# Performance work log

Hardware: AMD Instinct MI355X
Metric: run time of the kernel (lower is better)

The kernel has to match this reference:

```python
import jax, jax.numpy as jnp
import numpy as np

B, C, H, W = 8, 512, 32, 32
NUM_HEADS = 8
WINDOW = 32
L = H * W
BN_EPS = 1e-5


def setup_inputs() -> dict:
    key = jax.random.key(0)
    ks = jax.random.split(key, 8)
    s = lambda k, shape, sc=0.02: jax.random.normal(k, shape, jnp.float32) * sc
    return {
        "x": jax.random.normal(ks[0], (B, C, H, W), jnp.float32),
        "dw_weight": s(ks[1], (C, 1, 3, 3), 0.1),
        "dw_bias": jnp.zeros((C,), jnp.float32),
        "shared_weight": s(ks[2], (1, 1, 3, 3), 0.3),
        "shared_bias": jnp.zeros((1,), jnp.float32),
        "mix_weight": jnp.float32(0.7),
        "bn_gamma": jnp.ones((C,), jnp.float32),
        "bn_beta": jnp.zeros((C,), jnp.float32),
        "det_w1": s(ks[3], (C // 4, 2 * C)),
        "det_b1": jnp.zeros((C // 4,), jnp.float32),
        "det_w2": s(ks[4], (1, C // 4)),
        "det_b2": jnp.zeros((1,), jnp.float32),
        "in_proj_w": s(ks[5], (3 * C, C)),
        "in_proj_b": jnp.zeros((3 * C,), jnp.float32),
        "out_proj_w": s(ks[6], (C, C)),
        "out_proj_b": jnp.zeros((C,), jnp.float32),
    }


def _circ_pad(x):
    # F.pad(x, (1,1,1,1), mode='circular')
    return jnp.pad(x, ((0, 0), (0, 0), (1, 1), (1, 1)), mode="wrap")


def _dw_conv(xp, w, b):
    # depthwise 3x3, VALID on circularly padded input
    out = jax.lax.conv_general_dilated(
        xp, w, window_strides=(1, 1), padding="VALID",
        dimension_numbers=("NCHW", "OIHW", "NCHW"), feature_group_count=C)
    return out + b[None, :, None, None]


def _local_mask():
    # True = blocked; row i allows columns [i - WINDOW//2, i + WINDOW//2]
    i = jnp.arange(L)[:, None]
    j = jnp.arange(L)[None, :]
    allowed = (j >= i - WINDOW // 2) & (j <= i + WINDOW // 2)
    return ~allowed


def _forward(x, dw_weight, dw_bias, shared_weight, shared_bias, mix_weight,
             bn_gamma, bn_beta, det_w1, det_b1, det_w2, det_b2,
             in_proj_w, in_proj_b, out_proj_w, out_proj_b):
    # --- DualWalze (eval mode: BN uses running_mean=0, running_var=1) ---
    xp = _circ_pad(x)
    main_out = _dw_conv(xp, dw_weight, dw_bias)
    shared_kernel = jnp.broadcast_to(shared_weight, (C, 1, 3, 3))
    shared_b = jnp.broadcast_to(shared_bias, (C,))
    express_out = _dw_conv(xp, shared_kernel, shared_b)
    mix = jax.nn.sigmoid(mix_weight)
    combined = mix * main_out + (1.0 - mix) * express_out + x  # residual
    bn = bn_gamma[None, :, None, None] * combined * jax.lax.rsqrt(jnp.float32(1.0 + BN_EPS)) \
         + bn_beta[None, :, None, None]
    x_walze = jax.nn.gelu(bn, approximate=False)  # (B, C, H, W)

    # --- AdaptiveSpikeDetectorV3 (eval: no history, temp = 1.0) ---
    x_before_seq = x.transpose(0, 2, 3, 1).reshape(B, L, C)
    x_after_seq = x_walze.transpose(0, 2, 3, 1).reshape(B, L, C)
    comb = jnp.concatenate([x_before_seq, x_after_seq], axis=-1)  # (B, L, 2C)
    h = jax.nn.gelu(jnp.einsum("blf,kf->blk", comb, det_w1) + det_b1, approximate=False)
    spike_logits = jnp.einsum("blk,ok->blo", h, det_w2) + det_b2  # (B, L, 1)
    soft_mask = jax.nn.sigmoid(spike_logits)  # temperature 1.0 at progress 0
    soft_mask = soft_mask.reshape(B, H, W, 1).transpose(0, 3, 1, 2)  # (B,1,H,W)

    # --- AttentionWithMemory: windowed MHA over flattened sequence ---
    seq = x_after_seq  # (B, L, C)
    qkv = jnp.einsum("blc,fc->blf", seq, in_proj_w) + in_proj_b
    q, k, v = jnp.split(qkv, 3, axis=-1)
    hd = C // NUM_HEADS
    to_heads = lambda t: t.reshape(B, L, NUM_HEADS, hd).transpose(0, 2, 1, 3)
    q, k, v = to_heads(q), to_heads(k), to_heads(v)
    scores = jnp.einsum("bhqd,bhkd->bhqk", q, k) / jnp.sqrt(jnp.float32(hd))
    scores = jnp.where(_local_mask()[None, None], jnp.float32(-1e30), scores)
    attn = jax.nn.softmax(scores, axis=-1)
    ctx = jnp.einsum("bhqk,bhkd->bhqd", attn, v)
    ctx = ctx.transpose(0, 2, 1, 3).reshape(B, L, C)
    attn_out = jnp.einsum("blc,oc->blo", ctx, out_proj_w) + out_proj_b
    attn_spatial = attn_out.reshape(B, H, W, C).transpose(0, 3, 1, 2)

    # --- gated residual combine ---
    return x_walze + soft_mask * attn_spatial


def reference(x, dw_weight, dw_bias, shared_weight, shared_bias, mix_weight,
              bn_gamma, bn_beta, det_w1, det_b1, det_w2, det_b2,
              in_proj_w, in_proj_b, out_proj_w, out_proj_b):
    return _forward(x, dw_weight, dw_bias, shared_weight, shared_bias, mix_weight,
                    bn_gamma, bn_beta, det_w1, det_b1, det_w2, det_b2,
                    in_proj_w, in_proj_b, out_proj_w, out_proj_b)
```

## Files before the change

### kernel.cpp

```cpp
#include <hip/hip_runtime.h>

#define B_ 8
#define C_ 512
#define H_ 32
#define W_ 32
#define L_ 1024
#define M_ 8192
#define NH_ 8
#define HD_ 64

typedef float f32x4 __attribute__((ext_vector_type(4)));
typedef short s16x8 __attribute__((ext_vector_type(8)));

__device__ __forceinline__ f32x4 mfma_bf16(f32x4 acc, s16x8 a, s16x8 b) {
    asm("v_mfma_f32_16x16x32_bf16 %0, %1, %2, %0" : "+v"(acc) : "v"(a), "v"(b));
    return acc;
}

__device__ __forceinline__ s16x8 ldg8(const unsigned short* p) {
    return *(const s16x8*)p;
}

typedef __attribute__((address_space(1))) const unsigned int glob_u32;
typedef __attribute__((address_space(3))) unsigned int lds_u32;
__device__ __forceinline__ void async_cp16(const void* g, void* l) {
    __builtin_amdgcn_global_load_lds((glob_u32*)g, (lds_u32*)l, 16, 0, 0);
}

__device__ __forceinline__ unsigned short f2bf(float f) {
    unsigned int u = __float_as_uint(f);
    unsigned int r = (u + 0x7FFFu + ((u >> 16) & 1u)) >> 16;
    return (unsigned short)r;
}

__device__ __forceinline__ float bf2f(unsigned short u) {
    return __uint_as_float(((unsigned int)u) << 16);
}

__device__ __forceinline__ float gelu_exact(float v) {
    return 0.5f * v * (1.0f + erff(v * 0.70710678118654752f));
}

__device__ __forceinline__ float sigmoidf_(float v) {
    return 1.0f / (1.0f + __expf(-v));
}

__global__ __launch_bounds__(256) void k_cvt_weights(
        const float* __restrict__ w1, const float* __restrict__ w2,
        const float* __restrict__ w3,
        unsigned short* __restrict__ o1, unsigned short* __restrict__ o2,
        unsigned short* __restrict__ o3, int n1, int n2, int n3) {
    int i = blockIdx.x * 256 + threadIdx.x;
    if (i < n1) o1[i] = f2bf(w1[i]);
    if (i < n2) o2[i] = f2bf(w2[i]);
    if (i < n3) o3[i] = f2bf(w3[i]);
}

__global__ __launch_bounds__(256) void k_walze(
        const float* __restrict__ x, const float* __restrict__ dww,
        const float* __restrict__ dwb, const float* __restrict__ shw,
        const float* __restrict__ shb, const float* __restrict__ mixw,
        const float* __restrict__ gamma, const float* __restrict__ beta,
        float* __restrict__ xw) {
    __shared__ float tile[1024];
    int bc = blockIdx.x;
    int c = bc & (C_ - 1);
    int tid = threadIdx.x;
    const float* xp = x + (size_t)bc * 1024;
#pragma unroll
    for (int t = 0; t < 4; ++t) tile[tid + 256 * t] = xp[tid + 256 * t];
    __syncthreads();
    float wm[9], wsh[9];
#pragma unroll
    for (int t = 0; t < 9; ++t) { wm[t] = dww[c * 9 + t]; wsh[t] = shw[t]; }
    float mix = sigmoidf_(mixw[0]);
    float bmain = dwb[c], bsh = shb[0];
    float g = gamma[c], bt = beta[c];
    const float rs = rsqrtf(1.0f + 1e-5f);
#pragma unroll
    for (int t = 0; t < 4; ++t) {
        int l = tid + 256 * t;
        int h = l >> 5, w = l & 31;
        float accm = 0.f, accs = 0.f;
#pragma unroll
        for (int kh = 0; kh < 3; ++kh) {
            int hh = (h + kh + 31) & 31;
#pragma unroll
            for (int kw = 0; kw < 3; ++kw) {
                int ww = (w + kw + 31) & 31;
                float v = tile[hh * 32 + ww];
                accm += v * wm[kh * 3 + kw];
                accs += v * wsh[kh * 3 + kw];
            }
        }
        float combined = mix * (accm + bmain) + (1.f - mix) * (accs + bsh) + tile[l];
        float bn = g * combined * rs + bt;
        xw[(size_t)bc * 1024 + l] = gelu_exact(bn);
    }
}

__global__ __launch_bounds__(256) void k_pack(
        const float* __restrict__ x, const float* __restrict__ xw,
        unsigned short* __restrict__ comb) {
    __shared__ float Tx[64 * 65];
    __shared__ float Tw[64 * 65];
    int b = blockIdx.z;
    int c0 = blockIdx.y * 64;
    int l0 = blockIdx.x * 64;
    int tid = threadIdx.x;
    for (int idx = tid; idx < 1024; idx += 256) {
        int cr = idx >> 4, f = idx & 15;
        size_t src = ((size_t)(b * C_ + c0 + cr) << 10) + l0 + f * 4;
        float4 vx = *(const float4*)(x + src);
        float4 vw = *(const float4*)(xw + src);
        *(float4*)&Tx[cr * 65 + f * 4] = vx;
        *(float4*)&Tw[cr * 65 + f * 4] = vw;
    }
    __syncthreads();
    for (int idx = tid; idx < 1024; idx += 256) {
        int lr = idx >> 4, f = idx & 15;
        ushort4 ux, uw;
        ux.x = f2bf(Tx[(4 * f + 0) * 65 + lr]);
        ux.y = f2bf(Tx[(4 * f + 1) * 65 + lr]);
        ux.z = f2bf(Tx[(4 * f + 2) * 65 + lr]);
        ux.w = f2bf(Tx[(4 * f + 3) * 65 + lr]);
        uw.x = f2bf(Tw[(4 * f + 0) * 65 + lr]);
        uw.y = f2bf(Tw[(4 * f + 1) * 65 + lr]);
        uw.z = f2bf(Tw[(4 * f + 2) * 65 + lr]);
        uw.w = f2bf(Tw[(4 * f + 3) * 65 + lr]);
        unsigned short* row = comb + (((size_t)(b << 10) + l0 + lr) << 10);
        *(ushort4*)(row + c0 + 4 * f) = ux;
        *(ushort4*)(row + 512 + c0 + 4 * f) = uw;
    }
}

__global__ __launch_bounds__(256) void k_detector(
        const unsigned short* __restrict__ comb, const unsigned short* __restrict__ w1,
        const float* __restrict__ b1, const float* __restrict__ w2,
        const float* __restrict__ b2, float* __restrict__ sm) {
    __shared__ float red[64];
    int tid = threadIdx.x;
    int wave = tid >> 6, lane = tid & 63;
    int col = lane & 15, quad = lane >> 4;
    int m0 = blockIdx.x * 16;
    int koff = quad * 8;
    int nb0 = wave * 32, nb1 = nb0 + 16;
    const unsigned short* pa  = comb + (size_t)(m0 + col) * 1024 + koff;
    const unsigned short* pw0 = w1 + (size_t)(nb0 + col) * 1024 + koff;
    const unsigned short* pw1 = w1 + (size_t)(nb1 + col) * 1024 + koff;
    f32x4 acc0 = {0.f, 0.f, 0.f, 0.f}, acc1 = {0.f, 0.f, 0.f, 0.f};
    for (int k = 0; k < 1024; k += 32) {
        s16x8 a = ldg8(pa + k);
        acc0 = mfma_bf16(acc0, a, ldg8(pw0 + k));
        acc1 = mfma_bf16(acc1, a, ldg8(pw1 + k));
    }
    asm volatile("s_nop 7\ns_nop 7");
    float bia0 = b1[nb0 + col], bia1 = b1[nb1 + col];
    float wv0 = w2[nb0 + col], wv1 = w2[nb1 + col];
#pragma unroll
    for (int r = 0; r < 4; ++r) {
        float h0 = gelu_exact(acc0[r] + bia0);
        float h1 = gelu_exact(acc1[r] + bia1);
        float p = h0 * wv0 + h1 * wv1;
        p += __shfl_xor(p, 1);
        p += __shfl_xor(p, 2);
        p += __shfl_xor(p, 4);
        p += __shfl_xor(p, 8);
        if (col == 0) red[wave * 16 + quad * 4 + r] = p;
    }
    __syncthreads();
    if (tid < 16) {
        float s = red[tid] + red[16 + tid] + red[32 + tid] + red[48 + tid] + b2[0];
        sm[m0 + tid] = sigmoidf_(s);
    }
}

__global__ __launch_bounds__(256) void k_gemm_qkv(
        const unsigned short* __restrict__ A,
        const unsigned short* __restrict__ Wt,
        const float* __restrict__ bias,
        unsigned short* __restrict__ out_hi, unsigned short* __restrict__ out_lo) {
    __shared__ unsigned short As[128 * 64];
    __shared__ unsigned short Bs[128 * 64];
    int tid = threadIdx.x;
    int wave = tid >> 6, lane = tid & 63;
    int col = lane & 15, quad = lane >> 4;
    int wr = wave & 1, wc = wave >> 1;
    int mb = blockIdx.y * 128, nb = blockIdx.x * 128;
    int srow = tid >> 3, sko = tid & 7;
    f32x4 acc[4][4] = {};
    for (int kb = 0; kb < 512; kb += 64) {
#pragma unroll
        for (int p = 0; p < 4; ++p) {
            int r = p * 32 + srow;
            async_cp16(A + (size_t)(mb + r) * 1024 + kb + sko * 8, &As[r * 64 + sko * 8]);
            async_cp16(Wt + (size_t)(nb + r) * 512 + kb + sko * 8, &Bs[r * 64 + sko * 8]);
        }
        __syncthreads();
#pragma unroll
        for (int ks = 0; ks < 64; ks += 32) {
            s16x8 a[4], b[4];
#pragma unroll
            for (int i = 0; i < 4; ++i)
                a[i] = *(const s16x8*)&As[(wr * 64 + i * 16 + col) * 64 + ks + quad * 8];
#pragma unroll
            for (int j = 0; j < 4; ++j)
                b[j] = *(const s16x8*)&Bs[(wc * 64 + j * 16 + col) * 64 + ks + quad * 8];
#pragma unroll
            for (int i = 0; i < 4; ++i)
#pragma unroll
                for (int j = 0; j < 4; ++j)
                    acc[i][j] = mfma_bf16(acc[i][j], a[i], b[j]);
        }
        __syncthreads();
    }
    asm volatile("s_nop 7\ns_nop 7");
#pragma unroll
    for (int i = 0; i < 4; ++i)
#pragma unroll
        for (int j = 0; j < 4; ++j) {
            int n = nb + wc * 64 + j * 16 + col;
            float bv = bias[n];
#pragma unroll
            for (int r = 0; r < 4; ++r) {
                int m = mb + wr * 64 + i * 16 + quad * 4 + r;
                float v = acc[i][j][r] + bv;
                unsigned short hi = f2bf(v);
                size_t idx = (size_t)m * 1536 + n;
                out_hi[idx] = hi;
                out_lo[idx] = f2bf(v - bf2f(hi));
            }
        }
}

__global__ __launch_bounds__(256) void k_attn(
        const unsigned short* __restrict__ qkv_hi,
        const unsigned short* __restrict__ qkv_lo,
        unsigned short* __restrict__ ctx) {
    __shared__ unsigned short Vth[64 * 104];
    __shared__ unsigned short Vtl[64 * 104];
    __shared__ unsigned short Ph[4][16 * 104];
    __shared__ unsigned short Pl[4][16 * 104];
    int b = blockIdx.z, h = blockIdx.y;
    int q0 = blockIdx.x * 64;
    int tid = threadIdx.x, wave = tid >> 6, lane = tid & 63;
    int col = lane & 15, quad = lane >> 4;
    int jlo_t = max(q0 - 16, 0);
    const unsigned short* baseh = qkv_hi + ((size_t)(b << 10)) * 1536;
    const unsigned short* basel = qkv_lo + ((size_t)(b << 10)) * 1536;
#pragma unroll
    for (int it = 0; it < 3; ++it) {
        int slot = it * 256 + tid;
        int kg = slot >> 6, d = slot & 63;
        int key0 = jlo_t + kg * 8;
        unsigned short eh[8], el[8];
#pragma unroll
        for (int t = 0; t < 8; ++t) {
            size_t ro = (size_t)min(key0 + t, 1023) * 1536 + 1024 + h * 64 + d;
            eh[t] = baseh[ro];
            el[t] = basel[ro];
        }
        ushort4 h0 = {eh[0], eh[1], eh[2], eh[3]}, h1 = {eh[4], eh[5], eh[6], eh[7]};
        ushort4 l0 = {el[0], el[1], el[2], el[3]}, l1 = {el[4], el[5], el[6], el[7]};
        *(ushort4*)&Vth[d * 104 + kg * 8] = h0;
        *(ushort4*)&Vth[d * 104 + kg * 8 + 4] = h1;
        *(ushort4*)&Vtl[d * 104 + kg * 8] = l0;
        *(ushort4*)&Vtl[d * 104 + kg * 8 + 4] = l1;
    }
    __syncthreads();
    size_t qoff = (size_t)(q0 + wave * 16 + col) * 1536 + h * 64;
    s16x8 aq0h = ldg8(baseh + qoff + quad * 8);
    s16x8 aq1h = ldg8(baseh + qoff + 32 + quad * 8);
    s16x8 aq0l = ldg8(basel + qoff + quad * 8);
    s16x8 aq1l = ldg8(basel + qoff + 32 + quad * 8);
    f32x4 S[6];
#pragma unroll
    for (int nt = 0; nt < 6; ++nt) {
        size_t koffb = (size_t)min(jlo_t + nt * 16 + col, 1023) * 1536 + 512 + h * 64;
        s16x8 kh0 = ldg8(baseh + koffb + quad * 8);
        s16x8 kh1 = ldg8(baseh + koffb + 32 + quad * 8);
        s16x8 kl0 = ldg8(basel + koffb + quad * 8);
        s16x8 kl1 = ldg8(basel + koffb + 32 + quad * 8);
        f32x4 z = {0.f, 0.f, 0.f, 0.f};
        z = mfma_bf16(z, aq0h, kh0);
        z = mfma_bf16(z, aq1h, kh1);
        z = mfma_bf16(z, aq0h, kl0);
        z = mfma_bf16(z, aq1h, kl1);
        z = mfma_bf16(z, aq0l, kh0);
        z = mfma_bf16(z, aq1l, kh1);
        S[nt] = z;
    }
    asm volatile("s_nop 7\ns_nop 7");
    int i_base = q0 + wave * 16 + quad * 4;
    float mx[4] = {-1e30f, -1e30f, -1e30f, -1e30f};
#pragma unroll
    for (int nt = 0; nt < 6; ++nt) {
        int j = jlo_t + nt * 16 + col;
#pragma unroll
        for (int r = 0; r < 4; ++r) {
            int i = i_base + r;
            bool ok = (j <= 1023) && (j >= i - 16) && (j <= i + 16);
            float s = ok ? S[nt][r] * 0.125f : -1e30f;
            S[nt][r] = s;
            mx[r] = fmaxf(mx[r], s);
        }
    }
#pragma unroll
    for (int r = 0; r < 4; ++r) {
        mx[r] = fmaxf(mx[r], __shfl_xor(mx[r], 1));
        mx[r] = fmaxf(mx[r], __shfl_xor(mx[r], 2));
        mx[r] = fmaxf(mx[r], __shfl_xor(mx[r], 4));
        mx[r] = fmaxf(mx[r], __shfl_xor(mx[r], 8));
    }
    float sum[4] = {0.f, 0.f, 0.f, 0.f};
#pragma unroll
    for (int nt = 0; nt < 6; ++nt)
#pragma unroll
        for (int r = 0; r < 4; ++r) {
            float p = __expf(S[nt][r] - mx[r]);
            S[nt][r] = p;
            sum[r] += p;
        }
#pragma unroll
    for (int r = 0; r < 4; ++r) {
        sum[r] += __shfl_xor(sum[r], 1);
        sum[r] += __shfl_xor(sum[r], 2);
        sum[r] += __shfl_xor(sum[r], 4);
        sum[r] += __shfl_xor(sum[r], 8);
        sum[r] = 1.f / sum[r];
    }
#pragma unroll
    for (int nt = 0; nt < 6; ++nt)
#pragma unroll
        for (int r = 0; r < 4; ++r) {
            float pv = S[nt][r] * sum[r];
            unsigned short hi = f2bf(pv);
            Ph[wave][(quad * 4 + r) * 104 + nt * 16 + col] = hi;
            Pl[wave][(quad * 4 + r) * 104 + nt * 16 + col] = f2bf(pv - bf2f(hi));
        }
    __syncthreads();
    f32x4 O[4] = {};
#pragma unroll
    for (int ks = 0; ks < 96; ks += 32) {
        s16x8 aph = *(const s16x8*)&Ph[wave][col * 104 + ks + quad * 8];
        s16x8 apl = *(const s16x8*)&Pl[wave][col * 104 + ks + quad * 8];
#pragma unroll
        for (int nt = 0; nt < 4; ++nt) {
            s16x8 bvh = *(const s16x8*)&Vth[(nt * 16 + col) * 104 + ks + quad * 8];
            s16x8 bvl = *(const s16x8*)&Vtl[(nt * 16 + col) * 104 + ks + quad * 8];
            O[nt] = mfma_bf16(O[nt], aph, bvh);
            O[nt] = mfma_bf16(O[nt], apl, bvh);
            O[nt] = mfma_bf16(O[nt], aph, bvl);
        }
    }
    asm volatile("s_nop 7\ns_nop 7");
#pragma unroll
    for (int nt = 0; nt < 4; ++nt)
#pragma unroll
        for (int r = 0; r < 4; ++r) {
            int i = i_base + r;
            ctx[((size_t)(b << 10) + i) * 512 + h * 64 + nt * 16 + col] = f2bf(O[nt][r]);
        }
}

__global__ __launch_bounds__(256) void k_out_combine(
        const unsigned short* __restrict__ Wt, const unsigned short* __restrict__ Actx,
        const float* __restrict__ bias, const float* __restrict__ xw,
        const float* __restrict__ sm, float* __restrict__ out) {
    __shared__ unsigned short As[128 * 64];
    __shared__ unsigned short Bs[128 * 64];
    int tid = threadIdx.x;
    int wave = tid >> 6, lane = tid & 63;
    int col = lane & 15, quad = lane >> 4;
    int wr = wave & 1, wc = wave >> 1;
    int mb = blockIdx.y * 128, nb = blockIdx.x * 128;
    int srow = tid >> 3, sko = tid & 7;
    f32x4 acc[4][4] = {};
    for (int kb = 0; kb < 512; kb += 64) {
#pragma unroll
        for (int p = 0; p < 4; ++p) {
            int r = p * 32 + srow;
            async_cp16(Wt + (size_t)(mb + r) * 512 + kb + sko * 8, &As[r * 64 + sko * 8]);
            async_cp16(Actx + (size_t)(nb + r) * 512 + kb + sko * 8, &Bs[r * 64 + sko * 8]);
        }
        __syncthreads();
#pragma unroll
        for (int ks = 0; ks < 64; ks += 32) {
            s16x8 a[4], b[4];
#pragma unroll
            for (int i = 0; i < 4; ++i)
                a[i] = *(const s16x8*)&As[(wr * 64 + i * 16 + col) * 64 + ks + quad * 8];
#pragma unroll
            for (int j = 0; j < 4; ++j)
                b[j] = *(const s16x8*)&Bs[(wc * 64 + j * 16 + col) * 64 + ks + quad * 8];
#pragma unroll
            for (int i = 0; i < 4; ++i)
#pragma unroll
                for (int j = 0; j < 4; ++j)
                    acc[i][j] = mfma_bf16(acc[i][j], a[i], b[j]);
        }
        __syncthreads();
    }
    asm volatile("s_nop 7\ns_nop 7");
#pragma unroll
    for (int i = 0; i < 4; ++i)
#pragma unroll
        for (int j = 0; j < 4; ++j) {
            int seq = nb + wc * 64 + j * 16 + col;
            int bb = seq >> 10, l = seq & 1023;
            float smv = sm[seq];
#pragma unroll
            for (int r = 0; r < 4; ++r) {
                int c = mb + wr * 64 + i * 16 + quad * 4 + r;
                float v = acc[i][j][r] + bias[c];
                size_t oidx = ((size_t)(bb * C_ + c) << 10) + l;
                out[oidx] = xw[oidx] + smv * v;
            }
        }
}

extern "C" void kernel_launch(void* const* d_in, const int* in_sizes, int n_in,
                              void* d_out, int out_size, void* d_ws, size_t ws_size,
                              hipStream_t stream) {
    const float* x      = (const float*)d_in[0];
    const float* dw_w   = (const float*)d_in[1];
    const float* dw_b   = (const float*)d_in[2];
    const float* sh_w   = (const float*)d_in[3];
    const float* sh_b   = (const float*)d_in[4];
    const float* mix_w  = (const float*)d_in[5];
    const float* bn_g   = (const float*)d_in[6];
    const float* bn_b   = (const float*)d_in[7];
    const float* det_w1 = (const float*)d_in[8];
    const float* det_b1 = (const float*)d_in[9];
    const float* det_w2 = (const float*)d_in[10];
    const float* det_b2 = (const float*)d_in[11];
    const float* inp_w  = (const float*)d_in[12];
    const float* inp_b  = (const float*)d_in[13];
    const float* outp_w = (const float*)d_in[14];
    const float* outp_b = (const float*)d_in[15];
    float* out = (float*)d_out;

    char* ws = (char*)d_ws;
    size_t off = 0;
    auto alloc = [&](size_t bytes) -> void* {
        void* p = ws + off;
        off += (bytes + 255) & ~(size_t)255;
        return p;
    };
    float* xw             = (float*)alloc((size_t)M_ * C_ * 4);
    unsigned short* comb  = (unsigned short*)alloc((size_t)M_ * 1024 * 2);
    unsigned short* qkvh  = (unsigned short*)alloc((size_t)M_ * 1536 * 2);
    unsigned short* qkvl  = (unsigned short*)alloc((size_t)M_ * 1536 * 2);
    unsigned short* ctx   = (unsigned short*)alloc((size_t)M_ * 512 * 2);
    float* smask          = (float*)alloc((size_t)M_ * 4);
    unsigned short* w1b   = (unsigned short*)alloc(131072 * 2);
    unsigned short* inwb  = (unsigned short*)alloc(786432 * 2);
    unsigned short* outwb = (unsigned short*)alloc(262144 * 2);
    (void)ws_size; (void)in_sizes; (void)n_in; (void)out_size;

    k_cvt_weights<<<3072, 256, 0, stream>>>(det_w1, inp_w, outp_w, w1b, inwb, outwb,
                                            131072, 786432, 262144);
    k_walze<<<B_ * C_, 256, 0, stream>>>(x, dw_w, dw_b, sh_w, sh_b, mix_w, bn_g, bn_b, xw);
    k_pack<<<dim3(16, 8, 8), 256, 0, stream>>>(x, xw, comb);
    k_detector<<<M_ / 16, 256, 0, stream>>>(comb, w1b, det_b1, det_w2, det_b2, smask);
    k_gemm_qkv<<<dim3(1536 / 128, M_ / 128), 256, 0, stream>>>(comb + 512, inwb, inp_b,
                                                               qkvh, qkvl);
    k_attn<<<dim3(16, NH_, B_), 256, 0, stream>>>(qkvh, qkvl, ctx);
    k_out_combine<<<dim3(M_ / 128, C_ / 128), 256, 0, stream>>>(outwb, ctx, outp_b,
                                                                xw, smask, out);
}
```

Baseline: 197.4 us.

## Fuse depthwise-conv walze with bf16 pack and widen detector to 8 waves

Merges the depthwise-conv/BN/GELU kernel with the transpose-and-pack kernel. Each block loads a 4-row by 64-channel tile with circular halo rows into LDS, computes the walze output per channel lane, writes the bf16 combined rows directly, and writes xw back through an LDS transpose. This removes one launch and the re-read of x and xw from global memory. Separately, the detector kernel now uses 512 threads, each wave owning one 16-column N tile instead of two, to increase parallelism. The fused kernel's per-lane 2-byte strided comb stores and 32-entry register array may limit coalescing and occupancy.

```diff
diff --git a/kernel.cpp b/kernel.cpp
--- a/kernel.cpp
+++ b/kernel.cpp
@@ -56,20 +56,39 @@
     if (i < n3) o3[i] = f2bf(w3[i]);
 }
 
-__global__ __launch_bounds__(256) void k_walze(
+__global__ __launch_bounds__(256) void k_walze_pack(
         const float* __restrict__ x, const float* __restrict__ dww,
         const float* __restrict__ dwb, const float* __restrict__ shw,
         const float* __restrict__ shb, const float* __restrict__ mixw,
         const float* __restrict__ gamma, const float* __restrict__ beta,
-        float* __restrict__ xw) {
-    __shared__ float tile[1024];
-    int bc = blockIdx.x;
-    int c = bc & (C_ - 1);
+        float* __restrict__ xw, unsigned short* __restrict__ comb) {
+    __shared__ float lds[64 * 193];
+    int h0 = blockIdx.x * 4;
+    int c0 = blockIdx.y * 64;
+    int b  = blockIdx.z;
     int tid = threadIdx.x;
-    const float* xp = x + (size_t)bc * 1024;
-#pragma unroll
-    for (int t = 0; t < 4; ++t) tile[tid + 256 * t] = xp[tid + 256 * t];
-    __syncthreads();
+    const float* xb = x + ((size_t)(b * C_ + c0) << 10);
+#pragma unroll
+    for (int k = 0; k < 8; ++k) {
+        int idx = k * 256 + tid;
+        int c = idx >> 5, f = idx & 31;
+        float4 v = *(const float4*)(xb + ((size_t)c << 10) + h0 * 32 + f * 4);
+        *(float4*)&lds[c * 193 + 32 + f * 4] = v;
+    }
+    int hm1 = (h0 + 31) & 31, hp4 = (h0 + 4) & 31;
+#pragma unroll
+    for (int k = 0; k < 4; ++k) {
+        int idx = k * 256 + tid;
+        int c = idx >> 4, s = idx & 15;
+        int hi = s >> 3, f = s & 7;
+        int srow = hi ? hp4 : hm1;
+        float4 v = *(const float4*)(xb + ((size_t)c << 10) + srow * 32 + f * 4);
+        *(float4*)&lds[c * 193 + (hi ? 5 * 32 : 0) + f * 4] = v;
+    }
+    __syncthreads();
+    int lane = tid & 63;
+    int wave = tid >> 6;
+    int c = c0 + lane;
     float wm[9], wsh[9];
 #pragma unroll
     for (int t = 0; t < 9; ++t) { wm[t] = dww[c * 9 + t]; wsh[t] = shw[t]; }
@@ -77,100 +96,77 @@
     float bmain = dwb[c], bsh = shb[0];
     float g = gamma[c], bt = beta[c];
     const float rs = rsqrtf(1.0f + 1e-5f);
-#pragma unroll
-    for (int t = 0; t < 4; ++t) {
-        int l = tid + 256 * t;
-        int h = l >> 5, w = l & 31;
+    const float* myt = &lds[lane * 193];
+    int l_row = h0 * 32 + wave * 32;
+    unsigned short* crow = comb + (((size_t)(b << 10) + l_row) << 10);
+    float vreg[32];
+#pragma unroll
+    for (int w = 0; w < 32; ++w) {
         float accm = 0.f, accs = 0.f;
 #pragma unroll
         for (int kh = 0; kh < 3; ++kh) {
-            int hh = (h + kh + 31) & 31;
+            int tr = wave + kh;
 #pragma unroll
             for (int kw = 0; kw < 3; ++kw) {
                 int ww = (w + kw + 31) & 31;
-                float v = tile[hh * 32 + ww];
+                float v = myt[tr * 32 + ww];
                 accm += v * wm[kh * 3 + kw];
                 accs += v * wsh[kh * 3 + kw];
             }
         }
-        float combined = mix * (accm + bmain) + (1.f - mix) * (accs + bsh) + tile[l];
-        float bn = g * combined * rs + bt;
-        xw[(size_t)bc * 1024 + l] = gelu_exact(bn);
-    }
-}
-
-__global__ __launch_bounds__(256) void k_pack(
-        const float* __restrict__ x, const float* __restrict__ xw,
-        unsigned short* __restrict__ comb) {
-    __shared__ float Tx[64 * 65];
-    __shared__ float Tw[64 * 65];
-    int b = blockIdx.z;
-    int c0 = blockIdx.y * 64;
-    int l0 = blockIdx.x * 64;
-    int tid = threadIdx.x;
-    for (int idx = tid; idx < 1024; idx += 256) {
-        int cr = idx >> 4, f = idx & 15;
-        size_t src = ((size_t)(b * C_ + c0 + cr) << 10) + l0 + f * 4;
-        float4 vx = *(const float4*)(x + src);
-        float4 vw = *(const float4*)(xw + src);
-        *(float4*)&Tx[cr * 65 + f * 4] = vx;
-        *(float4*)&Tw[cr * 65 + f * 4] = vw;
-    }
-    __syncthreads();
-    for (int idx = tid; idx < 1024; idx += 256) {
-        int lr = idx >> 4, f = idx & 15;
-        ushort4 ux, uw;
-        ux.x = f2bf(Tx[(4 * f + 0) * 65 + lr]);
-        ux.y = f2bf(Tx[(4 * f + 1) * 65 + lr]);
-        ux.z = f2bf(Tx[(4 * f + 2) * 65 + lr]);
-        ux.w = f2bf(Tx[(4 * f + 3) * 65 + lr]);
-        uw.x = f2bf(Tw[(4 * f + 0) * 65 + lr]);
-        uw.y = f2bf(Tw[(4 * f + 1) * 65 + lr]);
-        uw.z = f2bf(Tw[(4 * f + 2) * 65 + lr]);
-        uw.w = f2bf(Tw[(4 * f + 3) * 65 + lr]);
-        unsigned short* row = comb + (((size_t)(b << 10) + l0 + lr) << 10);
-        *(ushort4*)(row + c0 + 4 * f) = ux;
-        *(ushort4*)(row + 512 + c0 + 4 * f) = uw;
-    }
-}
-
-__global__ __launch_bounds__(256) void k_detector(
+        float xo = myt[(wave + 1) * 32 + w];
+        float combined = mix * (accm + bmain) + (1.f - mix) * (accs + bsh) + xo;
+        float val = gelu_exact(g * combined * rs + bt);
+        vreg[w] = val;
+        crow[(size_t)w * 1024 + c0 + lane] = f2bf(xo);
+        crow[(size_t)w * 1024 + 512 + c0 + lane] = f2bf(val);
+    }
+    __syncthreads();
+#pragma unroll
+    for (int w = 0; w < 32; ++w)
+        lds[lane * 129 + wave * 32 + w] = vreg[w];
+    __syncthreads();
+#pragma unroll
+    for (int k = 0; k < 8; ++k) {
+        int idx = k * 256 + tid;
+        int cc = idx >> 5, f = idx & 31;
+        float4 v = *(const float4*)&lds[cc * 129 + f * 4];
+        *(float4*)(xw + ((size_t)(b * C_ + c0 + cc) << 10) + h0 * 32 + f * 4) = v;
+    }
+}
+
+__global__ __launch_bounds__(512) void k_detector(
         const unsigned short* __restrict__ comb, const unsigned short* __restrict__ w1,
         const float* __restrict__ b1, const float* __restrict__ w2,
         const float* __restrict__ b2, float* __restrict__ sm) {
-    __shared__ float red[64];
+    __shared__ float red[8][16];
     int tid = threadIdx.x;
     int wave = tid >> 6, lane = tid & 63;
     int col = lane & 15, quad = lane >> 4;
     int m0 = blockIdx.x * 16;
     int koff = quad * 8;
-    int nb0 = wave * 32, nb1 = nb0 + 16;
-    const unsigned short* pa  = comb + (size_t)(m0 + col) * 1024 + koff;
-    const unsigned short* pw0 = w1 + (size_t)(nb0 + col) * 1024 + koff;
-    const unsigned short* pw1 = w1 + (size_t)(nb1 + col) * 1024 + koff;
-    f32x4 acc0 = {0.f, 0.f, 0.f, 0.f}, acc1 = {0.f, 0.f, 0.f, 0.f};
-    for (int k = 0; k < 1024; k += 32) {
-        s16x8 a = ldg8(pa + k);
-        acc0 = mfma_bf16(acc0, a, ldg8(pw0 + k));
-        acc1 = mfma_bf16(acc1, a, ldg8(pw1 + k));
-    }
+    int nb = wave * 16;
+    const unsigned short* pa = comb + (size_t)(m0 + col) * 1024 + koff;
+    const unsigned short* pw = w1 + (size_t)(nb + col) * 1024 + koff;
+    f32x4 acc = {0.f, 0.f, 0.f, 0.f};
+    for (int k = 0; k < 1024; k += 32)
+        acc = mfma_bf16(acc, ldg8(pa + k), ldg8(pw + k));
     asm volatile("s_nop 7\ns_nop 7");
-    float bia0 = b1[nb0 + col], bia1 = b1[nb1 + col];
-    float wv0 = w2[nb0 + col], wv1 = w2[nb1 + col];
+    float bia = b1[nb + col], wv = w2[nb + col];
 #pragma unroll
     for (int r = 0; r < 4; ++r) {
-        float h0 = gelu_exact(acc0[r] + bia0);
-        float h1 = gelu_exact(acc1[r] + bia1);
-        float p = h0 * wv0 + h1 * wv1;
+        float p = gelu_exact(acc[r] + bia) * wv;
         p += __shfl_xor(p, 1);
         p += __shfl_xor(p, 2);
         p += __shfl_xor(p, 4);
         p += __shfl_xor(p, 8);
-        if (col == 0) red[wave * 16 + quad * 4 + r] = p;
+        if (col == 0) red[wave][quad * 4 + r] = p;
     }
     __syncthreads();
     if (tid < 16) {
-        float s = red[tid] + red[16 + tid] + red[32 + tid] + red[48 + tid] + b2[0];
+        float s = b2[0];
+#pragma unroll
+        for (int w = 0; w < 8; ++w) s += red[w][tid];
         sm[m0 + tid] = sigmoidf_(s);
     }
 }
@@ -460,9 +456,9 @@
 
     k_cvt_weights<<<3072, 256, 0, stream>>>(det_w1, inp_w, outp_w, w1b, inwb, outwb,
                                             131072, 786432, 262144);
-    k_walze<<<B_ * C_, 256, 0, stream>>>(x, dw_w, dw_b, sh_w, sh_b, mix_w, bn_g, bn_b, xw);
-    k_pack<<<dim3(16, 8, 8), 256, 0, stream>>>(x, xw, comb);
-    k_detector<<<M_ / 16, 256, 0, stream>>>(comb, w1b, det_b1, det_w2, det_b2, smask);
+    k_walze_pack<<<dim3(8, 8, 8), 256, 0, stream>>>(x, dw_w, dw_b, sh_w, sh_b, mix_w,
+                                                    bn_g, bn_b, xw, comb);
+    k_detector<<<M_ / 16, 512, 0, stream>>>(comb, w1b, det_b1, det_w2, det_b2, smask);
     k_gemm_qkv<<<dim3(1536 / 128, M_ / 128), 256, 0, stream>>>(comb + 512, inwb, inp_b,
                                                                qkvh, qkvl);
     k_attn<<<dim3(16, NH_, B_), 256, 0, stream>>>(qkvh, qkvl, ctx);
```

Result: slower. 202.6 us (+2.6%).
